# Kernel tuning notes

Hardware: AMD Instinct MI355X
Metric: run time of the kernel (lower is better)

Reference implementation:

```python
import jax, jax.numpy as jnp
import numpy as np
import math

V_RANGE = 1
SHIFTS = [(x, y) for x in range(-V_RANGE, V_RANGE + 1) for y in range(-V_RANGE, V_RANGE + 1)]


def circ_conv(x, w, b=None):
    # Conv2d with circular padding, NCHW / OIHW layout.
    p = w.shape[-1] // 2
    xp = jnp.pad(x, ((0, 0), (0, 0), (p, p), (p, p)), mode='wrap')
    y = jax.lax.conv_general_dilated(xp, w, (1, 1), 'VALID',
                                     dimension_numbers=('NCHW', 'OIHW', 'NCHW'))
    if b is not None:
        y = y + b[None, :, None, None]
    return y


def setup_inputs() -> dict:
    key = jax.random.key(0)
    ks = jax.random.split(key, 6)
    B, d_model, d_state, H, W = 4, 64, 16, 32, 32
    num_v = (2 * V_RANGE + 1) ** 2  # 9
    return {
        'u_t': jax.random.normal(ks[0], (B, d_model, H, W), jnp.float32),
        's_prev': jax.random.normal(ks[1], (B, num_v, d_model, d_state, H, W), jnp.float32),
        'W_delta': jax.random.normal(ks[2], (d_model, d_model, 3, 3), jnp.float32) * 0.05,
        'b_delta': jnp.zeros((d_model,), jnp.float32),
        'W_B': jax.random.normal(ks[3], (d_state, d_model, 3, 3), jnp.float32) * 0.05,
        'W_C': jax.random.normal(ks[4], (d_state, d_model, 3, 3), jnp.float32) * 0.05,
        'log_A_real': jnp.log(0.5 * jnp.ones((d_model, d_state), jnp.float32)),
        'D': jnp.ones((d_model,), jnp.float32),
        'dt_inv_softplus': jnp.float32(math.log(math.e - 1.0)),
    }


def reference(u_t, s_prev, W_delta, b_delta, W_B, W_C, log_A_real, D, dt_inv_softplus):
    # Parameter generation from input
    delta = jax.nn.softplus(circ_conv(u_t, W_delta, b_delta) + dt_inv_softplus)  # (B,d,H,W)
    B_val = circ_conv(u_t, W_B)  # (B,n,H,W)
    C_val = circ_conv(u_t, W_C)  # (B,n,H,W)

    # ZOH discretization (pointwise)
    A = -jnp.exp(log_A_real)                         # (d,n)
    A_bc = A[None, :, :, None, None]                 # (1,d,n,1,1)
    A_bar = jnp.exp(delta[:, :, None] * A_bc)        # (B,d,n,H,W)
    B_bar = (A_bar - 1.0) / A_bc * B_val[:, None]    # (B,d,n,H,W)
    bu = B_bar * u_t[:, :, None]                     # (B,d,n,H,W)

    # Transport: per-velocity spatial roll, vectorized with vmap over the V axis
    vx = jnp.array([s[0] for s in SHIFTS])
    vy = jnp.array([s[1] for s in SHIFTS])
    roll_v = jax.vmap(lambda s, x, y: jnp.roll(s, shift=(-y, -x), axis=(-2, -1)),
                      in_axes=(1, 0, 0), out_axes=1)
    s_trans = roll_v(s_prev, vx, vy)                 # (B,V,d,n,H,W)

    # State update and output
    s_next = A_bar[:, None] * s_trans + bu[:, None]  # (B,V,d,n,H,W)
    y_state = jnp.sum(s_next * C_val[:, None, None], axis=3)  # (B,V,d,H,W)
    y_out = y_state + (u_t * D[None, :, None, None])[:, None]
    return y_out, s_next
```

## Files before the change

### kernel.cpp

```cpp
#include <hip/hip_runtime.h>
#include <math.h>

#define B_   4
#define DM   64
#define DS   16
#define HW_  1024
#define NV   9

typedef float f32x4 __attribute__((ext_vector_type(4)));

#define Y_SIZE   2359296
#define WS_DELTA 0
#define WS_BV    (B_*DM*HW_)
#define WS_CV    (WS_BV + B_*DS*HW_)

__global__ __launch_bounds__(256) void conv_kernel(
    const float* __restrict__ u,
    const float* __restrict__ Wd,
    const float* __restrict__ bd,
    const float* __restrict__ Wb,
    const float* __restrict__ Wc,
    const float* __restrict__ dtp,
    float* __restrict__ ws)
{
    __shared__ float su[8 * 320];
    __shared__ float sw[DM * 9 * 8];

    const int bid = blockIdx.x;
    const int b   = bid / 48;
    const int r   = bid % 48;
    const int g   = r >> 2;
    const int h0  = (r & 3) * 8;
    const int co0 = g * 8;

    const float* Wsrc;
    int cbase, mode;
    if (co0 < 64)      { Wsrc = Wd; cbase = co0;      mode = 0; }
    else if (co0 < 80) { Wsrc = Wb; cbase = co0 - 64; mode = 1; }
    else               { Wsrc = Wc; cbase = co0 - 80; mode = 2; }

    const int tid = threadIdx.x;

    for (int i = tid; i < DM * 9 * 8; i += 256) {
        const int j  = i & 7;
        const int ct = i >> 3;
        sw[i] = Wsrc[(cbase + j) * 576 + ct];
    }

    const int hl = tid >> 5;
    const int w  = tid & 31;
    const int pix = ((h0 + hl) << 5) | w;

    float acc[8];
    #pragma unroll
    for (int j = 0; j < 8; ++j) acc[j] = 0.f;
    const float* ub = u + (size_t)b * DM * HW_;

    for (int c0 = 0; c0 < DM; c0 += 8) {
        __syncthreads();
        #pragma unroll
        for (int k = 0; k < 10; ++k) {
            const int i   = k * 256 + tid;
            const int cl  = i / 320;
            const int pos = i - cl * 320;
            const int rr  = pos >> 5;
            su[i] = ub[(c0 + cl) * HW_ + ((((h0 - 1 + rr) & 31) << 5) | (pos & 31))];
        }
        __syncthreads();
        #pragma unroll
        for (int cl = 0; cl < 8; ++cl) {
            #pragma unroll
            for (int kh = 0; kh < 3; ++kh) {
                const int rs = hl + kh;
                #pragma unroll
                for (int kw = 0; kw < 3; ++kw) {
                    const int ww = (w + kw + 31) & 31;
                    const float v = su[cl * 320 + ((rs << 5) | ww)];
                    const int wb = ((c0 + cl) * 9 + kh * 3 + kw) * 8;
                    const float4 w0 = *(const float4*)&sw[wb];
                    const float4 w1 = *(const float4*)&sw[wb + 4];
                    acc[0] = fmaf(v, w0.x, acc[0]);
                    acc[1] = fmaf(v, w0.y, acc[1]);
                    acc[2] = fmaf(v, w0.z, acc[2]);
                    acc[3] = fmaf(v, w0.w, acc[3]);
                    acc[4] = fmaf(v, w1.x, acc[4]);
                    acc[5] = fmaf(v, w1.y, acc[5]);
                    acc[6] = fmaf(v, w1.z, acc[6]);
                    acc[7] = fmaf(v, w1.w, acc[7]);
                }
            }
        }
    }

    if (mode == 0) {
        const float dt = dtp[0];
        #pragma unroll
        for (int j = 0; j < 8; ++j) {
            const float x  = acc[j] + bd[cbase + j] + dt;
            const float sp = fmaxf(x, 0.f) + log1pf(expf(-fabsf(x)));
            ws[WS_DELTA + ((size_t)b * DM + cbase + j) * HW_ + pix] = sp;
        }
    } else if (mode == 1) {
        #pragma unroll
        for (int j = 0; j < 8; ++j)
            ws[WS_BV + ((size_t)b * DS + cbase + j) * HW_ + pix] = acc[j];
    } else {
        #pragma unroll
        for (int j = 0; j < 8; ++j)
            ws[WS_CV + ((size_t)b * DS + cbase + j) * HW_ + pix] = acc[j];
    }
}

__global__ __launch_bounds__(512) void scan_kernel(
    const float* __restrict__ u,
    const float* __restrict__ s_prev,
    const float* __restrict__ logA,
    const float* __restrict__ Dv,
    const float* __restrict__ ws,
    float* __restrict__ out)
{
    const int bid  = blockIdx.x >> 1;
    const int half = blockIdx.x & 1;
    const int c   = bid & 63;
    const int bv  = bid >> 6;
    const int v   = bv % 9;
    const int b   = bv / 9;

    __shared__ float sAr[DS], sIr[DS];
    __shared__ float syl[4 * 512];

    const int tid = threadIdx.x;
    if (tid < DS) {
        const float A = -__expf(logA[(c << 4) + tid]);
        sAr[tid] = A;
        sIr[tid] = 1.0f / A;
    }
    __syncthreads();

    const int quad = tid & 127;
    const int nthr = tid >> 7;
    const int lane = tid & 63;

    const int hw4 = (half << 9) | (quad << 2);
    const int h   = hw4 >> 5;

    const int sx  = v / 3 - 1;
    const int syy = v % 3 - 1;
    const int hs  = (h + syy) & 31;
    const int rowbase = (hs << 5) | ((quad & 7) << 2);

    const int srcp = (lane & ~7) | ((lane + 1) & 7);
    const int srcm = (lane & ~7) | ((lane + 7) & 7);

    const int bc = (b << 6) | c;
    const float4 u4 = *(const float4*)&u[(bc << 10) | hw4];
    const float4 d4 = *(const float4*)&ws[WS_DELTA + ((bc << 10) | hw4)];

    const float* __restrict__ sp  = s_prev + ((size_t)bid << 14);
    float* __restrict__ so        = out + Y_SIZE + ((size_t)bid << 14);
    const float* __restrict__ bvp = ws + WS_BV + ((b << 14) | hw4);
    const float* __restrict__ cvp = ws + WS_CV + ((b << 14) | hw4);

    float4 spv[4], bvv[4], cvv[4];
    #pragma unroll
    for (int i = 0; i < 4; ++i) {
        const int n = (nthr << 2) + i;
        spv[i] = *(const float4*)&sp[(n << 10) + rowbase];
        bvv[i] = *(const float4*)&bvp[n << 10];
        cvv[i] = *(const float4*)&cvp[n << 10];
    }

    float4 acc = make_float4(0.f, 0.f, 0.f, 0.f);
    #pragma unroll
    for (int i = 0; i < 4; ++i) {
        const int n = (nthr << 2) + i;
        float4 sh;
        if (sx > 0) {
            const float edge = __shfl(spv[i].x, srcp);
            sh = make_float4(spv[i].y, spv[i].z, spv[i].w, edge);
        } else if (sx < 0) {
            const float edge = __shfl(spv[i].w, srcm);
            sh = make_float4(edge, spv[i].x, spv[i].y, spv[i].z);
        } else {
            sh = spv[i];
        }
        const float A  = sAr[n];
        const float iA = sIr[n];
        float4 e;
        f32x4 s;
        e.x = __expf(d4.x * A);
        e.y = __expf(d4.y * A);
        e.z = __expf(d4.z * A);
        e.w = __expf(d4.w * A);
        s.x = fmaf(e.x, sh.x, (e.x - 1.f) * iA * bvv[i].x * u4.x);
        s.y = fmaf(e.y, sh.y, (e.y - 1.f) * iA * bvv[i].y * u4.y);
        s.z = fmaf(e.z, sh.z, (e.z - 1.f) * iA * bvv[i].z * u4.z);
        s.w = fmaf(e.w, sh.w, (e.w - 1.f) * iA * bvv[i].w * u4.w);
        __builtin_nontemporal_store(s, (f32x4*)&so[(n << 10) + hw4]);
        acc.x = fmaf(s.x, cvv[i].x, acc.x);
        acc.y = fmaf(s.y, cvv[i].y, acc.y);
        acc.z = fmaf(s.z, cvv[i].z, acc.z);
        acc.w = fmaf(s.w, cvv[i].w, acc.w);
    }

    *(float4*)&syl[(nthr << 9) | (quad << 2)] = make_float4(acc.x, acc.y, acc.z, acc.w);
    __syncthreads();
    if (tid < 128) {
        const float4 a0 = *(const float4*)&syl[(0 << 9) | (tid << 2)];
        const float4 a1 = *(const float4*)&syl[(1 << 9) | (tid << 2)];
        const float4 a2 = *(const float4*)&syl[(2 << 9) | (tid << 2)];
        const float4 a3 = *(const float4*)&syl[(3 << 9) | (tid << 2)];
        const float Dc = Dv[c];
        f32x4 y;
        y.x = a0.x + a1.x + a2.x + a3.x + u4.x * Dc;
        y.y = a0.y + a1.y + a2.y + a3.y + u4.y * Dc;
        y.z = a0.z + a1.z + a2.z + a3.z + u4.z * Dc;
        y.w = a0.w + a1.w + a2.w + a3.w + u4.w * Dc;
        __builtin_nontemporal_store(y, (f32x4*)&out[(bid << 10) | hw4]);
    }
}

extern "C" void kernel_launch(void* const* d_in, const int* in_sizes, int n_in,
                              void* d_out, int out_size, void* d_ws, size_t ws_size,
                              hipStream_t stream) {
    const float* u      = (const float*)d_in[0];
    const float* s_prev = (const float*)d_in[1];
    const float* Wd     = (const float*)d_in[2];
    const float* bd     = (const float*)d_in[3];
    const float* Wb     = (const float*)d_in[4];
    const float* Wc     = (const float*)d_in[5];
    const float* logA   = (const float*)d_in[6];
    const float* Dv     = (const float*)d_in[7];
    const float* dtp    = (const float*)d_in[8];
    float* out = (float*)d_out;
    float* ws  = (float*)d_ws;

    conv_kernel<<<B_ * 12 * 4, 256, 0, stream>>>(u, Wd, bd, Wb, Wc, dtp, ws);
    scan_kernel<<<B_ * NV * DM * 2, 512, 0, stream>>>(u, s_prev, logA, Dv, ws, out);
}
```

Baseline: 73.25 us.

## Split conv over more blocks and process both halves per scan block

The conv kernel now computes 4 output channels per block instead of 8, doubling its grid from 192 to 384 blocks so more CUs are busy. The scan kernel now covers the full 1024-pixel plane per block, issuing all s_prev loads for both halves up front and running the second half's compute after the first. This halves the scan grid and amortises per-block setup, at the cost of more registers and fewer blocks.

```diff
diff --git a/kernel.cpp b/kernel.cpp
--- a/kernel.cpp
+++ b/kernel.cpp
@@ -24,14 +24,14 @@
     float* __restrict__ ws)
 {
     __shared__ float su[8 * 320];
-    __shared__ float sw[DM * 9 * 8];
+    __shared__ float sw[DM * 9 * 4];
 
     const int bid = blockIdx.x;
-    const int b   = bid / 48;
-    const int r   = bid % 48;
+    const int b   = bid / 96;
+    const int r   = bid % 96;
     const int g   = r >> 2;
     const int h0  = (r & 3) * 8;
-    const int co0 = g * 8;
+    const int co0 = g * 4;
 
     const float* Wsrc;
     int cbase, mode;
@@ -41,9 +41,9 @@
 
     const int tid = threadIdx.x;
 
-    for (int i = tid; i < DM * 9 * 8; i += 256) {
-        const int j  = i & 7;
-        const int ct = i >> 3;
+    for (int i = tid; i < DM * 9 * 4; i += 256) {
+        const int j  = i & 3;
+        const int ct = i >> 2;
         sw[i] = Wsrc[(cbase + j) * 576 + ct];
     }
 
@@ -51,9 +51,9 @@
     const int w  = tid & 31;
     const int pix = ((h0 + hl) << 5) | w;
 
-    float acc[8];
-    #pragma unroll
-    for (int j = 0; j < 8; ++j) acc[j] = 0.f;
+    float acc[4];
+    #pragma unroll
+    for (int j = 0; j < 4; ++j) acc[j] = 0.f;
     const float* ub = u + (size_t)b * DM * HW_;
 
     for (int c0 = 0; c0 < DM; c0 += 8) {
@@ -76,17 +76,11 @@
                 for (int kw = 0; kw < 3; ++kw) {
                     const int ww = (w + kw + 31) & 31;
                     const float v = su[cl * 320 + ((rs << 5) | ww)];
-                    const int wb = ((c0 + cl) * 9 + kh * 3 + kw) * 8;
-                    const float4 w0 = *(const float4*)&sw[wb];
-                    const float4 w1 = *(const float4*)&sw[wb + 4];
+                    const float4 w0 = *(const float4*)&sw[((c0 + cl) * 9 + kh * 3 + kw) * 4];
                     acc[0] = fmaf(v, w0.x, acc[0]);
                     acc[1] = fmaf(v, w0.y, acc[1]);
                     acc[2] = fmaf(v, w0.z, acc[2]);
                     acc[3] = fmaf(v, w0.w, acc[3]);
-                    acc[4] = fmaf(v, w1.x, acc[4]);
-                    acc[5] = fmaf(v, w1.y, acc[5]);
-                    acc[6] = fmaf(v, w1.z, acc[6]);
-                    acc[7] = fmaf(v, w1.w, acc[7]);
                 }
             }
         }
@@ -95,18 +89,18 @@
     if (mode == 0) {
         const float dt = dtp[0];
         #pragma unroll
-        for (int j = 0; j < 8; ++j) {
+        for (int j = 0; j < 4; ++j) {
             const float x  = acc[j] + bd[cbase + j] + dt;
             const float sp = fmaxf(x, 0.f) + log1pf(expf(-fabsf(x)));
             ws[WS_DELTA + ((size_t)b * DM + cbase + j) * HW_ + pix] = sp;
         }
     } else if (mode == 1) {
         #pragma unroll
-        for (int j = 0; j < 8; ++j)
+        for (int j = 0; j < 4; ++j)
             ws[WS_BV + ((size_t)b * DS + cbase + j) * HW_ + pix] = acc[j];
     } else {
         #pragma unroll
-        for (int j = 0; j < 8; ++j)
+        for (int j = 0; j < 4; ++j)
             ws[WS_CV + ((size_t)b * DS + cbase + j) * HW_ + pix] = acc[j];
     }
 }
@@ -119,15 +113,14 @@
     const float* __restrict__ ws,
     float* __restrict__ out)
 {
-    const int bid  = blockIdx.x >> 1;
-    const int half = blockIdx.x & 1;
+    const int bid = blockIdx.x;
     const int c   = bid & 63;
     const int bv  = bid >> 6;
     const int v   = bv % 9;
     const int b   = bv / 9;
 
     __shared__ float sAr[DS], sIr[DS];
-    __shared__ float syl[4 * 512];
+    __shared__ float syl[2 * 4 * 512];
 
     const int tid = threadIdx.x;
     if (tid < DS) {
@@ -140,83 +133,124 @@
     const int quad = tid & 127;
     const int nthr = tid >> 7;
     const int lane = tid & 63;
-
-    const int hw4 = (half << 9) | (quad << 2);
-    const int h   = hw4 >> 5;
+    const int nb   = nthr << 2;
 
     const int sx  = v / 3 - 1;
     const int syy = v % 3 - 1;
-    const int hs  = (h + syy) & 31;
-    const int rowbase = (hs << 5) | ((quad & 7) << 2);
+
+    const int hw0 = quad << 2;
+    const int hw1 = 512 | hw0;
+    const int h0t = hw0 >> 5;
+    const int hs0 = (h0t + syy) & 31;
+    const int hs1 = (h0t + 16 + syy) & 31;
+    const int colb = (quad & 7) << 2;
+    const int rb0 = (hs0 << 5) | colb;
+    const int rb1 = (hs1 << 5) | colb;
 
     const int srcp = (lane & ~7) | ((lane + 1) & 7);
     const int srcm = (lane & ~7) | ((lane + 7) & 7);
 
     const int bc = (b << 6) | c;
-    const float4 u4 = *(const float4*)&u[(bc << 10) | hw4];
-    const float4 d4 = *(const float4*)&ws[WS_DELTA + ((bc << 10) | hw4)];
-
     const float* __restrict__ sp  = s_prev + ((size_t)bid << 14);
     float* __restrict__ so        = out + Y_SIZE + ((size_t)bid << 14);
-    const float* __restrict__ bvp = ws + WS_BV + ((b << 14) | hw4);
-    const float* __restrict__ cvp = ws + WS_CV + ((b << 14) | hw4);
-
-    float4 spv[4], bvv[4], cvv[4];
+    const float* __restrict__ bvp = ws + WS_BV + (b << 14);
+    const float* __restrict__ cvp = ws + WS_CV + (b << 14);
+
+    float4 sp0[4], sp1[4], bv0[4], cv0[4];
+    #pragma unroll
+    for (int i = 0; i < 4; ++i)
+        sp0[i] = *(const float4*)&sp[((nb + i) << 10) + rb0];
+    #pragma unroll
+    for (int i = 0; i < 4; ++i)
+        sp1[i] = *(const float4*)&sp[((nb + i) << 10) + rb1];
     #pragma unroll
     for (int i = 0; i < 4; ++i) {
-        const int n = (nthr << 2) + i;
-        spv[i] = *(const float4*)&sp[(n << 10) + rowbase];
-        bvv[i] = *(const float4*)&bvp[n << 10];
-        cvv[i] = *(const float4*)&cvp[n << 10];
+        bv0[i] = *(const float4*)&bvp[((nb + i) << 10) + hw0];
+        cv0[i] = *(const float4*)&cvp[((nb + i) << 10) + hw0];
+    }
+    const float4 u40 = *(const float4*)&u[(bc << 10) | hw0];
+    const float4 d40 = *(const float4*)&ws[WS_DELTA + ((bc << 10) | hw0)];
+    const float4 u41 = *(const float4*)&u[(bc << 10) | hw1];
+    const float4 d41 = *(const float4*)&ws[WS_DELTA + ((bc << 10) | hw1)];
+
+#define COMPT(SPV, BVV, CVV, U4, D4, HW)                                   \
+    {                                                                      \
+        _Pragma("unroll")                                                  \
+        for (int i = 0; i < 4; ++i) {                                      \
+            const int n = nb + i;                                          \
+            float4 sh;                                                     \
+            if (sx > 0) {                                                  \
+                const float edge = __shfl(SPV[i].x, srcp);                 \
+                sh = make_float4(SPV[i].y, SPV[i].z, SPV[i].w, edge);      \
+            } else if (sx < 0) {                                           \
+                const float edge = __shfl(SPV[i].w, srcm);                 \
+                sh = make_float4(edge, SPV[i].x, SPV[i].y, SPV[i].z);      \
+            } else {                                                       \
+                sh = SPV[i];                                               \
+            }                                                              \
+            const float A  = sAr[n];                                       \
+            const float iA = sIr[n];                                       \
+            float4 e;                                                      \
+            f32x4 s;                                                       \
+            e.x = __expf(D4.x * A);                                        \
+            e.y = __expf(D4.y * A);                                        \
+            e.z = __expf(D4.z * A);                                        \
+            e.w = __expf(D4.w * A);                                        \
+            s.x = fmaf(e.x, sh.x, (e.x - 1.f) * iA * BVV[i].x * U4.x);     \
+            s.y = fmaf(e.y, sh.y, (e.y - 1.f) * iA * BVV[i].y * U4.y);     \
+            s.z = fmaf(e.z, sh.z, (e.z - 1.f) * iA * BVV[i].z * U4.z);     \
+            s.w = fmaf(e.w, sh.w, (e.w - 1.f) * iA * BVV[i].w * U4.w);     \
+            __builtin_nontemporal_store(s, (f32x4*)&so[(n << 10) + (HW)]); \
+            acc.x = fmaf(s.x, CVV[i].x, acc.x);                            \
+            acc.y = fmaf(s.y, CVV[i].y, acc.y);                            \
+            acc.z = fmaf(s.z, CVV[i].z, acc.z);                            \
+            acc.w = fmaf(s.w, CVV[i].w, acc.w);                            \
+        }                                                                  \
     }
 
     float4 acc = make_float4(0.f, 0.f, 0.f, 0.f);
+    COMPT(sp0, bv0, cv0, u40, d40, hw0);
+    *(float4*)&syl[(nthr << 9) | (quad << 2)] = acc;
+
+    float4 bv1[4], cv1[4];
     #pragma unroll
     for (int i = 0; i < 4; ++i) {
-        const int n = (nthr << 2) + i;
-        float4 sh;
-        if (sx > 0) {
-            const float edge = __shfl(spv[i].x, srcp);
-            sh = make_float4(spv[i].y, spv[i].z, spv[i].w, edge);
-        } else if (sx < 0) {
-            const float edge = __shfl(spv[i].w, srcm);
-            sh = make_float4(edge, spv[i].x, spv[i].y, spv[i].z);
-        } else {
-            sh = spv[i];
-        }
-        const float A  = sAr[n];
-        const float iA = sIr[n];
-        float4 e;
-        f32x4 s;
-        e.x = __expf(d4.x * A);
-        e.y = __expf(d4.y * A);
-        e.z = __expf(d4.z * A);
-        e.w = __expf(d4.w * A);
-        s.x = fmaf(e.x, sh.x, (e.x - 1.f) * iA * bvv[i].x * u4.x);
-        s.y = fmaf(e.y, sh.y, (e.y - 1.f) * iA * bvv[i].y * u4.y);
-        s.z = fmaf(e.z, sh.z, (e.z - 1.f) * iA * bvv[i].z * u4.z);
-        s.w = fmaf(e.w, sh.w, (e.w - 1.f) * iA * bvv[i].w * u4.w);
-        __builtin_nontemporal_store(s, (f32x4*)&so[(n << 10) + hw4]);
-        acc.x = fmaf(s.x, cvv[i].x, acc.x);
-        acc.y = fmaf(s.y, cvv[i].y, acc.y);
-        acc.z = fmaf(s.z, cvv[i].z, acc.z);
-        acc.w = fmaf(s.w, cvv[i].w, acc.w);
-    }
-
-    *(float4*)&syl[(nthr << 9) | (quad << 2)] = make_float4(acc.x, acc.y, acc.z, acc.w);
+        bv1[i] = *(const float4*)&bvp[((nb + i) << 10) + hw1];
+        cv1[i] = *(const float4*)&cvp[((nb + i) << 10) + hw1];
+    }
+
+    acc = make_float4(0.f, 0.f, 0.f, 0.f);
+    COMPT(sp1, bv1, cv1, u41, d41, hw1);
+    *(float4*)&syl[2048 + ((nthr << 9) | (quad << 2))] = acc;
+
+#undef COMPT
+
     __syncthreads();
+
+    const float Dc = Dv[c];
     if (tid < 128) {
         const float4 a0 = *(const float4*)&syl[(0 << 9) | (tid << 2)];
         const float4 a1 = *(const float4*)&syl[(1 << 9) | (tid << 2)];
         const float4 a2 = *(const float4*)&syl[(2 << 9) | (tid << 2)];
         const float4 a3 = *(const float4*)&syl[(3 << 9) | (tid << 2)];
-        const float Dc = Dv[c];
         f32x4 y;
-        y.x = a0.x + a1.x + a2.x + a3.x + u4.x * Dc;
-        y.y = a0.y + a1.y + a2.y + a3.y + u4.y * Dc;
-        y.z = a0.z + a1.z + a2.z + a3.z + u4.z * Dc;
-        y.w = a0.w + a1.w + a2.w + a3.w + u4.w * Dc;
-        __builtin_nontemporal_store(y, (f32x4*)&out[(bid << 10) | hw4]);
+        y.x = a0.x + a1.x + a2.x + a3.x + u40.x * Dc;
+        y.y = a0.y + a1.y + a2.y + a3.y + u40.y * Dc;
+        y.z = a0.z + a1.z + a2.z + a3.z + u40.z * Dc;
+        y.w = a0.w + a1.w + a2.w + a3.w + u40.w * Dc;
+        __builtin_nontemporal_store(y, (f32x4*)&out[(bid << 10) | (tid << 2)]);
+    } else if (tid < 256) {
+        const int qq = tid & 127;
+        const float4 a0 = *(const float4*)&syl[2048 + (0 << 9) + (qq << 2)];
+        const float4 a1 = *(const float4*)&syl[2048 + (1 << 9) + (qq << 2)];
+        const float4 a2 = *(const float4*)&syl[2048 + (2 << 9) + (qq << 2)];
+        const float4 a3 = *(const float4*)&syl[2048 + (3 << 9) + (qq << 2)];
+        f32x4 y;
+        y.x = a0.x + a1.x + a2.x + a3.x + u41.x * Dc;
+        y.y = a0.y + a1.y + a2.y + a3.y + u41.y * Dc;
+        y.z = a0.z + a1.z + a2.z + a3.z + u41.z * Dc;
+        y.w = a0.w + a1.w + a2.w + a3.w + u41.w * Dc;
+        __builtin_nontemporal_store(y, (f32x4*)&out[(bid << 10) | 512 | (qq << 2)]);
     }
 }
 
@@ -235,6 +269,6 @@
     float* out = (float*)d_out;
     float* ws  = (float*)d_ws;
 
-    conv_kernel<<<B_ * 12 * 4, 256, 0, stream>>>(u, Wd, bd, Wb, Wc, dtp, ws);
-    scan_kernel<<<B_ * NV * DM * 2, 512, 0, stream>>>(u, s_prev, logA, Dv, ws, out);
+    conv_kernel<<<B_ * 24 * 4, 256, 0, stream>>>(u, Wd, bd, Wb, Wc, dtp, ws);
+    scan_kernel<<<B_ * NV * DM, 512, 0, stream>>>(u, s_prev, logA, Dv, ws, out);
 }
```

New measurement: 77.95 us. +6.4%, slower.
